# Performance work log

Hardware: AMD Instinct MI355X
Metric: run time of the kernel (lower is better)

## Reference

```python
import jax, jax.numpy as jnp
import numpy as np

B, N, F, I = 4, 1024, 32, 8
DIM, DN, NF = 256, 64, 100
H, HD = 4, 64  # heads, head_dim (H*HD == DIM)
EPS = 1e-5


def setup_inputs() -> dict:
    key = jax.random.key(0)
    ks = jax.random.split(key, 24)
    def p(k, shape, s=0.05):
        return jax.random.normal(k, shape, jnp.float32) * s
    return {
        "x": jax.random.normal(ks[0], (B, N, F, I), jnp.float32),
        "idx": jax.random.randint(ks[1], (F,), 0, NF),
        "ctx": jax.random.normal(ks[2], (B, 1, DN), jnp.float32),
        "Wp": p(ks[3], (NF, DIM * I)),          # in_projection table
        "Bp": p(ks[4], (NF, DIM)),               # feature_bias table
        "q_emb": p(ks[5], (1, DIM)),             # queries table
        "cln_kv_W": p(ks[6], (DN, 2 * DIM)), "cln_kv_b": jnp.zeros((2 * DIM,), jnp.float32),
        "cln_q_W": p(ks[7], (DN, 2 * DIM)),  "cln_q_b": jnp.zeros((2 * DIM,), jnp.float32),
        "cln_h_W": p(ks[8], (DN, 2 * DIM)),  "cln_h_b": jnp.zeros((2 * DIM,), jnp.float32),
        "Wq": p(ks[9], (DIM, DIM)), "Wk": p(ks[10], (DIM, DIM)),
        "Wv": p(ks[11], (DIM, DIM)), "Wo": p(ks[12], (DIM, DIM)),
        "W1": p(ks[13], (DIM, 4 * DIM)), "b1": jnp.zeros((4 * DIM,), jnp.float32),
        "W2": p(ks[14], (4 * DIM, DIM)), "b2": jnp.zeros((DIM,), jnp.float32),
    }


def _ln(x):
    m = x.mean(-1, keepdims=True)
    v = ((x - m) ** 2).mean(-1, keepdims=True)
    return (x - m) * jax.lax.rsqrt(v + EPS)


def _cln(x, c, W, b):
    # adaptive layernorm: ln(x) * (1 + scale(ctx)) + shift(ctx)
    h = _ln(x)
    s, sh = jnp.split(c @ W + b, 2, axis=-1)
    return h * (1.0 + s) + sh


def reference(x, idx, ctx, Wp, Bp, q_emb, cln_kv_W, cln_kv_b, cln_q_W, cln_q_b,
              cln_h_W, cln_h_b, Wq, Wk, Wv, Wo, W1, b1, W2, b2):
    b_, n_, f_, i_ = x.shape
    # gather per-feature projection weights and biases
    w = Wp[idx].reshape(f_, DIM, i_)                 # [f, d, i]
    bias = Bp[idx][None]                              # [1, f, d] (broadcasts b,n)
    kv = jnp.einsum('bnfi,fdi->bnfd', x, w)           # [b, n, f, d]
    c = ctx[:, :, None, :]                            # [b, 1, 1, dn]
    kv = _cln(kv, c, cln_kv_W, cln_kv_b) + bias
    q = jnp.broadcast_to(q_emb[None, None], (b_, n_, 1, DIM))
    # cross-attention (pre-norm, conditional)
    qn = _cln(q, c, cln_q_W, cln_q_b)
    qh = (qn @ Wq).reshape(b_, n_, 1, H, HD)
    kh = (kv @ Wk).reshape(b_, n_, f_, H, HD)
    vh = (kv @ Wv).reshape(b_, n_, f_, H, HD)
    att = jnp.einsum('bnqhe,bnfhe->bnhqf', qh, kh) / np.sqrt(HD).astype(np.float32)
    att = jax.nn.softmax(att, axis=-1)
    o = jnp.einsum('bnhqf,bnfhe->bnqhe', att, vh).reshape(b_, n_, 1, DIM) @ Wo
    h = q + o
    # MLP (pre-norm, conditional)
    hn = _cln(h, c, cln_h_W, cln_h_b)
    h = h + (jax.nn.gelu(hn @ W1 + b1) @ W2 + b2)
    return h[:, :, 0, :]                              # squeeze query dim -> [b, n, d]
```

## Files before the change

kernel.cpp:

```cpp
#include <hip/hip_runtime.h>
#include <cmath>

#define EPSV 1e-5f
using f4 = float4;

typedef __attribute__((ext_vector_type(8))) short bfrag;
typedef __attribute__((ext_vector_type(4))) float ffrag;

#define WS_SKV   0
#define WS_SHKV  1024
#define WS_SH    2048
#define WS_SHH   3072
#define WS_A     4096
#define WS_R     8192
#define WS_HT    4202496
#define WS_G     6299648
#define WS_GB    WS_G
#define WS_HNB   (WS_G + 2097152)
#define WS_W1T   (WS_G + 2621440)
#define WS_W2T   (WS_G + 2752512)

#define FMA8(acc, s, wa, wb) \
  acc[0]=fmaf((s),(wa).x,acc[0]); acc[1]=fmaf((s),(wa).y,acc[1]); \
  acc[2]=fmaf((s),(wa).z,acc[2]); acc[3]=fmaf((s),(wa).w,acc[3]); \
  acc[4]=fmaf((s),(wb).x,acc[4]); acc[5]=fmaf((s),(wb).y,acc[5]); \
  acc[6]=fmaf((s),(wb).z,acc[6]); acc[7]=fmaf((s),(wb).w,acc[7]);

#define FMA4(acc, s, wa) \
  acc[0]=fmaf((s),(wa).x,acc[0]); acc[1]=fmaf((s),(wa).y,acc[1]); \
  acc[2]=fmaf((s),(wa).z,acc[2]); acc[3]=fmaf((s),(wa).w,acc[3]);

#define DOT8(res, v, wa, wb) \
  res = fmaf((v)[0],(wa).x,res); res = fmaf((v)[1],(wa).y,res); \
  res = fmaf((v)[2],(wa).z,res); res = fmaf((v)[3],(wa).w,res); \
  res = fmaf((v)[4],(wb).x,res); res = fmaf((v)[5],(wb).y,res); \
  res = fmaf((v)[6],(wb).z,res); res = fmaf((v)[7],(wb).w,res);

__device__ __forceinline__ float bfly32(float v){
  v += __shfl_xor(v, 1);  v += __shfl_xor(v, 2);  v += __shfl_xor(v, 4);
  v += __shfl_xor(v, 8);  v += __shfl_xor(v, 16);
  return v;
}

__device__ __forceinline__ float gelu_tanh(float x){
  float inner = 0.7978845608028654f*(x + 0.044715f*x*x*x);
  return 0.5f*x*(1.0f + tanhf(inner));
}
__device__ __forceinline__ float gelu_fast(float x){
  float z2 = 1.5957691216057308f*(x + 0.044715f*x*x*x);
  return x / (1.0f + __expf(-z2));
}

__device__ __forceinline__ unsigned short f2bf(float x){
  union { float f; unsigned u; } v; v.f = x;
  unsigned r = v.u + 0x7fffu + ((v.u >> 16) & 1u);
  return (unsigned short)(r >> 16);
}

__global__ __launch_bounds__(256) void kw_conv(
  const float* __restrict__ W1, const float* __restrict__ W2,
  float* __restrict__ ws)
{
  __shared__ unsigned short lt[64][68];
  const int tid = threadIdx.x;
  int blk = blockIdx.x;
  const float* src; unsigned short* dst; int K, N, K0, N0;
  if (blk < 64){
    src = W1; dst = (unsigned short*)(ws + WS_W1T);
    K = 256; N = 1024; K0 = (blk >> 4)*64; N0 = (blk & 15)*64;
  } else {
    blk -= 64;
    src = W2; dst = (unsigned short*)(ws + WS_W2T);
    K = 1024; N = 256; K0 = (blk >> 2)*64; N0 = (blk & 3)*64;
  }
  #pragma unroll
  for (int i=0;i<4;++i){
    int r = i*16 + (tid>>4);
    int c = (tid&15)*4;
    f4 v = *(const f4*)(src + (size_t)(K0+r)*N + N0 + c);
    lt[r][c]   = f2bf(v.x); lt[r][c+1] = f2bf(v.y);
    lt[r][c+2] = f2bf(v.z); lt[r][c+3] = f2bf(v.w);
  }
  __syncthreads();
  #pragma unroll
  for (int i=0;i<4;++i){
    int n  = i*16 + (tid>>4);
    int kc = (tid&15)*4;
    ushort4 u;
    u.x = lt[kc][n]; u.y = lt[kc+1][n]; u.z = lt[kc+2][n]; u.w = lt[kc+3][n];
    *(ushort4*)(dst + (size_t)(N0+n)*K + K0 + kc) = u;
  }
}

__global__ __launch_bounds__(256) void k0_all(
    const float* __restrict__ ctx, const float* __restrict__ q_emb,
    const float* __restrict__ Wkv, const float* __restrict__ bkv,
    const float* __restrict__ Wqc, const float* __restrict__ bqc,
    const float* __restrict__ Whc, const float* __restrict__ bhc,
    const float* __restrict__ Wq,  const float* __restrict__ Wk,
    float* __restrict__ ws)
{
  const int b = blockIdx.x >> 2, h = blockIdx.x & 3;
  const int tid = threadIdx.x;
  __shared__ float c[64], qn[256], ph[256], qh64[64], red[8];
  if (tid < 64) c[tid] = ctx[b*64 + tid];
  __syncthreads();

  float skv = bkv[tid],      shkv = bkv[256+tid];
  float sq  = bqc[tid],      shq  = bqc[256+tid];
  float sh  = bhc[tid],      shh  = bhc[256+tid];
  #pragma unroll 8
  for (int j=0;j<64;++j){
    float cj = c[j];
    skv  = fmaf(cj, Wkv[j*512 + tid],       skv);
    shkv = fmaf(cj, Wkv[j*512 + 256 + tid], shkv);
    sq   = fmaf(cj, Wqc[j*512 + tid],       sq);
    shq  = fmaf(cj, Wqc[j*512 + 256 + tid], shq);
    sh   = fmaf(cj, Whc[j*512 + tid],       sh);
    shh  = fmaf(cj, Whc[j*512 + 256 + tid], shh);
  }
  if (h == 0){
    ws[WS_SKV  + b*256 + tid] = skv;
    ws[WS_SHKV + b*256 + tid] = shkv;
    ws[WS_SH   + b*256 + tid] = sh;
    ws[WS_SHH  + b*256 + tid] = shh;
  }

  float qe = q_emb[tid];
  float s1r = qe, s2r = qe*qe;
  for (int mm=1;mm<64;mm<<=1){ s1r += __shfl_xor(s1r,mm); s2r += __shfl_xor(s2r,mm); }
  int wv = tid>>6, ln = tid&63;
  if (ln==0){ red[wv*2]=s1r; red[wv*2+1]=s2r; }
  __syncthreads();
  float S1 = red[0]+red[2]+red[4]+red[6];
  float S2 = red[1]+red[3]+red[5]+red[7];
  float mean = S1*(1.0f/256.0f);
  float var  = S2*(1.0f/256.0f) - mean*mean;
  float rs   = rsqrtf(var + EPSV);
  qn[tid] = (qe-mean)*rs*(1.0f+sq) + shq;
  __syncthreads();

  {
    const int t = tid & 63, ks = tid >> 6;
    float p = 0.f;
    const float* wq = Wq + (size_t)(ks*64)*256 + h*64 + t;
    #pragma unroll 8
    for (int d=0; d<64; ++d) p = fmaf(qn[ks*64+d], wq[d*256], p);
    ph[tid] = p;
  }
  __syncthreads();
  if (tid < 64) qh64[tid] = ph[tid] + ph[64+tid] + ph[128+tid] + ph[192+tid];
  __syncthreads();

  {
    float a = 0.f;
    const float* wkr = Wk + (size_t)tid*256 + h*64;
    #pragma unroll
    for (int e4=0; e4<16; ++e4){
      f4 wv4 = *(const f4*)(wkr + e4*4);
      a = fmaf(qh64[e4*4+0], wv4.x, a);
      a = fmaf(qh64[e4*4+1], wv4.y, a);
      a = fmaf(qh64[e4*4+2], wv4.z, a);
      a = fmaf(qh64[e4*4+3], wv4.w, a);
    }
    ws[WS_A + b*1024 + h*256 + tid] = 0.125f*a;
  }
}

__global__ __launch_bounds__(256) void k1f_attn(
  const float* __restrict__ x, const int* __restrict__ idx,
  const float* __restrict__ Wp, const float* __restrict__ Bp,
  float* __restrict__ ws)
{
  __shared__ float xs[2048];
  __shared__ float wls[2][2048];
  __shared__ float As[1024];

  const int tid = threadIdx.x;
  const int p0  = blockIdx.x * 8;
  const int b   = p0 >> 10;
  const int t   = tid >> 5;
  const int dg  = tid & 31;
  const int dA  = 4*dg, dB = 128 + 4*dg;

  {
    const float* xg = x + (size_t)p0*256 + tid*8;
    f4 a  = *(const f4*)xg;
    f4 bq = *(const f4*)(xg + 4);
    *(f4*)&xs[tid*8]     = a;
    *(f4*)&xs[tid*8 + 4] = bq;
  }
  *(f4*)&As[tid*4] = *(const f4*)(ws + WS_A + b*1024 + tid*4);

  f4 skA = *(const f4*)(ws + WS_SKV  + b*256 + dA);
  f4 skB = *(const f4*)(ws + WS_SKV  + b*256 + dB);
  f4 shA = *(const f4*)(ws + WS_SHKV + b*256 + dA);
  f4 shB = *(const f4*)(ws + WS_SHKV + b*256 + dB);
  float coef[8] = {1.f+skA.x,1.f+skA.y,1.f+skA.z,1.f+skA.w,
                   1.f+skB.x,1.f+skB.y,1.f+skB.z,1.f+skB.w};
  float shk[8]  = {shA.x,shA.y,shA.z,shA.w, shB.x,shB.y,shB.z,shB.w};

  int row = idx[0];
  f4 u0, u1;
  {
    const float* wp0 = Wp + (size_t)row*2048 + tid*8;
    u0 = *(const f4*)wp0;
    u1 = *(const f4*)(wp0 + 4);
  }

  float l[4] = {0.f,0.f,0.f,0.f};
  float racc[4][8] = {};

  for (int f = 0; f < 32; ++f){
    {
      float* wb = wls[f&1];
      wb[0*256+tid]=u0.x; wb[1*256+tid]=u0.y; wb[2*256+tid]=u0.z; wb[3*256+tid]=u0.w;
      wb[4*256+tid]=u1.x; wb[5*256+tid]=u1.y; wb[6*256+tid]=u1.z; wb[7*256+tid]=u1.w;
    }
    f4 ba = *(const f4*)(Bp + (size_t)row*256 + dA);
    f4 bb = *(const f4*)(Bp + (size_t)row*256 + dB);
    int rown = idx[f < 31 ? f+1 : 31];
    const float* wpn = Wp + (size_t)rown*2048 + tid*8;
    row = rown;
    __syncthreads();
    u0 = *(const f4*)wpn;
    u1 = *(const f4*)(wpn + 4);

    f4 xa = *(const f4*)&xs[t*256 + f*8];
    f4 xb = *(const f4*)&xs[t*256 + f*8 + 4];
    float xf[8] = {xa.x,xa.y,xa.z,xa.w, xb.x,xb.y,xb.z,xb.w};

    float val[8] = {};
    const float* wrow = wls[f&1];
    #pragma unroll
    for (int i=0;i<8;++i){
      f4 wa = *(const f4*)&wrow[i*256 + dA];
      f4 wbv = *(const f4*)&wrow[i*256 + dB];
      FMA8(val, xf[i], wa, wbv);
    }

    float s=0.f, ss=0.f;
    #pragma unroll
    for (int jj=0;jj<8;++jj){ s += val[jj]; ss = fmaf(val[jj],val[jj],ss); }
    s = bfly32(s); ss = bfly32(ss);
    float mean = s*(1.f/256.f);
    float var  = ss*(1.f/256.f) - mean*mean;
    float rsg  = rsqrtf(var + EPSV);
    float mrs  = mean*rsg;

    float off[8] = {shk[0]+ba.x, shk[1]+ba.y, shk[2]+ba.z, shk[3]+ba.w,
                    shk[4]+bb.x, shk[5]+bb.y, shk[6]+bb.z, shk[7]+bb.w};
    float kvl[8];
    #pragma unroll
    for (int jj=0;jj<8;++jj)
      kvl[jj] = fmaf(fmaf(val[jj], rsg, -mrs), coef[jj], off[jj]);

    #pragma unroll
    for (int h=0;h<4;++h){
      f4 Aa = *(const f4*)&As[h*256 + dA];
      f4 Ab = *(const f4*)&As[h*256 + dB];
      float lg = 0.f;
      DOT8(lg, kvl, Aa, Ab);
      lg = bfly32(lg);
      float pp = __expf(lg);
      l[h] += pp;
      #pragma unroll
      for (int jj=0;jj<8;++jj)
        racc[h][jj] = fmaf(pp, kvl[jj], racc[h][jj]);
    }
  }

  float* rp = ws + WS_R + (size_t)(p0+t)*1024;
  #pragma unroll
  for (int h=0;h<4;++h){
    float inv = 1.f / l[h];
    *(f4*)&rp[h*256 + dA] = make_float4(racc[h][0]*inv, racc[h][1]*inv,
                                        racc[h][2]*inv, racc[h][3]*inv);
    *(f4*)&rp[h*256 + dB] = make_float4(racc[h][4]*inv, racc[h][5]*inv,
                                        racc[h][6]*inv, racc[h][7]*inv);
  }
}

__global__ __launch_bounds__(256) void k2_ovo(
  const float* __restrict__ Wv, const float* __restrict__ Wo,
  const float* __restrict__ q_emb, float* __restrict__ ws)
{
  __shared__ float rl[8192];
  __shared__ float ot[2048];
  __shared__ float wt[2][2048];

  const int tid = threadIdx.x;
  const int p0  = blockIdx.x * 8;
  const int b   = p0 >> 10;
  const int tq  = tid >> 5;
  const int jq  = tid & 31;
  const int cA  = 4*jq, cB = 128 + 4*jq;
  const int hA  = jq >> 4, hB = 2 + (jq >> 4);

  #pragma unroll
  for (int i=0;i<8;++i){
    int off = i*1024 + tid*4;
    *(f4*)&rl[off] = *(const f4*)(ws + WS_R + (size_t)p0*1024 + off);
  }

  const int q0 = tid, q1 = tid + 256;
  f4 uw0, uw1;
  uw0 = *(const f4*)(Wv + (size_t)(q0>>6)*256 + (q0&63)*4);
  uw1 = *(const f4*)(Wv + (size_t)(q1>>6)*256 + (q1&63)*4);

  float oa[8] = {};
  for (int c=0; c<32; ++c){
    float* wb = wt[c&1];
    *(f4*)&wb[(q0>>6)*256 + (q0&63)*4] = uw0;
    *(f4*)&wb[(q1>>6)*256 + (q1&63)*4] = uw1;
    __syncthreads();
    int cn = (c < 31) ? c+1 : 31;
    uw0 = *(const f4*)(Wv + (size_t)(cn*8 + (q0>>6))*256 + (q0&63)*4);
    uw1 = *(const f4*)(Wv + (size_t)(cn*8 + (q1>>6))*256 + (q1&63)*4);
    const float* wrow = wt[c&1];
    #pragma unroll
    for (int dd=0; dd<8; ++dd){
      int d = c*8 + dd;
      float rA = rl[tq*1024 + hA*256 + d];
      float rB = rl[tq*1024 + hB*256 + d];
      f4 w0 = *(const f4*)&wrow[dd*256 + cA];
      f4 w1 = *(const f4*)&wrow[dd*256 + cB];
      FMA4(oa, rA, w0);
      float* ob4 = oa + 4;
      FMA4(ob4, rB, w1);
    }
  }
  *(f4*)&ot[tq*256 + cA] = make_float4(oa[0],oa[1],oa[2],oa[3]);
  *(f4*)&ot[tq*256 + cB] = make_float4(oa[4],oa[5],oa[6],oa[7]);
  uw0 = *(const f4*)(Wo + (size_t)(q0>>6)*256 + (q0&63)*4);
  uw1 = *(const f4*)(Wo + (size_t)(q1>>6)*256 + (q1&63)*4);
  __syncthreads();

  float ob[8] = {};
  for (int c=0; c<32; ++c){
    float* wb = wt[c&1];
    *(f4*)&wb[(q0>>6)*256 + (q0&63)*4] = uw0;
    *(f4*)&wb[(q1>>6)*256 + (q1&63)*4] = uw1;
    __syncthreads();
    int cn = (c < 31) ? c+1 : 31;
    uw0 = *(const f4*)(Wo + (size_t)(cn*8 + (q0>>6))*256 + (q0&63)*4);
    uw1 = *(const f4*)(Wo + (size_t)(cn*8 + (q1>>6))*256 + (q1&63)*4);
    const float* wrow = wt[c&1];
    #pragma unroll
    for (int dd=0; dd<8; ++dd){
      int cc = c*8 + dd;
      float a = ot[tq*256 + cc];
      f4 w0 = *(const f4*)&wrow[dd*256 + cA];
      f4 w1 = *(const f4*)&wrow[dd*256 + cB];
      FMA8(ob, a, w0, w1);
    }
  }

  f4 qA = *(const f4*)(q_emb + cA);
  f4 qB = *(const f4*)(q_emb + cB);
  float ht[8] = {ob[0]+qA.x, ob[1]+qA.y, ob[2]+qA.z, ob[3]+qA.w,
                 ob[4]+qB.x, ob[5]+qB.y, ob[6]+qB.z, ob[7]+qB.w};
  float s=0.f, ss=0.f;
  #pragma unroll
  for (int jj=0;jj<8;++jj){ s += ht[jj]; ss = fmaf(ht[jj],ht[jj],ss); }
  s = bfly32(s); ss = bfly32(ss);
  float mean = s*(1.f/256.f);
  float var  = ss*(1.f/256.f) - mean*mean;
  float rsg  = rsqrtf(var + EPSV);
  f4 sH0 = *(const f4*)(ws + WS_SH  + b*256 + cA);
  f4 sH1 = *(const f4*)(ws + WS_SH  + b*256 + cB);
  f4 hH0 = *(const f4*)(ws + WS_SHH + b*256 + cA);
  f4 hH1 = *(const f4*)(ws + WS_SHH + b*256 + cB);
  float sHv[8]  = {sH0.x,sH0.y,sH0.z,sH0.w, sH1.x,sH1.y,sH1.z,sH1.w};
  float hHv[8]  = {hH0.x,hH0.y,hH0.z,hH0.w, hH1.x,hH1.y,hH1.z,hH1.w};
  float hnv[8];
  #pragma unroll
  for (int jj=0;jj<8;++jj)
    hnv[jj] = (ht[jj]-mean)*rsg*(1.f+sHv[jj]) + hHv[jj];

  float* htp = ws + WS_HT + (size_t)(p0+tq)*256;
  *(f4*)(htp+cA) = make_float4(ht[0],ht[1],ht[2],ht[3]);
  *(f4*)(htp+cB) = make_float4(ht[4],ht[5],ht[6],ht[7]);
  unsigned short* hnb = (unsigned short*)(ws + WS_HNB);
  ushort4 uA, uB;
  uA.x=f2bf(hnv[0]); uA.y=f2bf(hnv[1]); uA.z=f2bf(hnv[2]); uA.w=f2bf(hnv[3]);
  uB.x=f2bf(hnv[4]); uB.y=f2bf(hnv[5]); uB.z=f2bf(hnv[6]); uB.w=f2bf(hnv[7]);
  *(ushort4*)(hnb + (size_t)(p0+tq)*256 + cA) = uA;
  *(ushort4*)(hnb + (size_t)(p0+tq)*256 + cB) = uB;
}

__global__ __launch_bounds__(256) void k3_mfma(
  const float* __restrict__ b1, float* __restrict__ ws)
{
  __shared__ unsigned short aT[2][64*40];
  __shared__ unsigned short bT[2][128*40];
  const unsigned short* hnb = (const unsigned short*)(ws + WS_HNB);
  const unsigned short* w1t = (const unsigned short*)(ws + WS_W1T);
  unsigned short* gb = (unsigned short*)(ws + WS_GB);

  const int tid = threadIdx.x;
  const int M0 = (blockIdx.x >> 3) * 64;
  const int N0 = (blockIdx.x & 7) * 128;
  const int lane = tid & 63;
  const int wid = tid >> 6;
  const int wm = wid >> 1, wn = wid & 1;
  const int m16 = lane & 15, q = lane >> 4;

  const int sa_m = tid >> 2, sa_k = (tid & 3) * 8;
  const int sb_n = tid >> 1, sb_k = (tid & 1) * 16;

  f4 ua, ub0, ub1;
  ua  = *(const f4*)(hnb + (size_t)(M0 + sa_m)*256 + sa_k);
  ub0 = *(const f4*)(w1t + (size_t)(N0 + sb_n)*256 + sb_k);
  ub1 = *(const f4*)(w1t + (size_t)(N0 + sb_n)*256 + sb_k + 8);

  ffrag acc[2][4];
  #pragma unroll
  for (int i=0;i<2;++i)
    #pragma unroll
    for (int j=0;j<4;++j) acc[i][j] = (ffrag){0.f,0.f,0.f,0.f};

  for (int ks=0; ks<8; ++ks){
    const int buf = ks & 1;
    *(f4*)&aT[buf][sa_m*40 + sa_k]     = ua;
    *(f4*)&bT[buf][sb_n*40 + sb_k]     = ub0;
    *(f4*)&bT[buf][sb_n*40 + sb_k + 8] = ub1;
    __syncthreads();
    int kn = (ks < 7) ? ks+1 : 7;
    ua  = *(const f4*)(hnb + (size_t)(M0 + sa_m)*256 + kn*32 + sa_k);
    ub0 = *(const f4*)(w1t + (size_t)(N0 + sb_n)*256 + kn*32 + sb_k);
    ub1 = *(const f4*)(w1t + (size_t)(N0 + sb_n)*256 + kn*32 + sb_k + 8);

    bfrag af[2], bf_[4];
    af[0] = *(const bfrag*)&aT[buf][(wm*32 + m16)*40 + q*8];
    af[1] = *(const bfrag*)&aT[buf][(wm*32 + 16 + m16)*40 + q*8];
    #pragma unroll
    for (int j=0;j<4;++j)
      bf_[j] = *(const bfrag*)&bT[buf][(wn*64 + j*16 + m16)*40 + q*8];
    #pragma unroll
    for (int i=0;i<2;++i)
      #pragma unroll
      for (int j=0;j<4;++j)
        acc[i][j] = __builtin_amdgcn_mfma_f32_16x16x32_bf16(bf_[j], af[i], acc[i][j], 0, 0, 0);
  }

  #pragma unroll
  for (int i=0;i<2;++i){
    const int m = M0 + wm*32 + i*16 + m16;
    #pragma unroll
    for (int j=0;j<4;++j){
      const int n4 = N0 + wn*64 + j*16 + q*4;
      f4 bv = *(const f4*)(b1 + n4);
      ushort4 u;
      u.x = f2bf(gelu_fast(acc[i][j][0] + bv.x));
      u.y = f2bf(gelu_fast(acc[i][j][1] + bv.y));
      u.z = f2bf(gelu_fast(acc[i][j][2] + bv.z));
      u.w = f2bf(gelu_fast(acc[i][j][3] + bv.w));
      *(ushort4*)(gb + (size_t)m*1024 + n4) = u;
    }
  }
}

__global__ __launch_bounds__(256) void k4_mfma(
  const float* __restrict__ b2, const float* __restrict__ ws_c,
  float* __restrict__ ws, float* __restrict__ out)
{
  __shared__ unsigned short aT[2][32*40];
  __shared__ unsigned short bT[2][64*40];
  const unsigned short* gb  = (const unsigned short*)(ws_c + WS_GB);
  const unsigned short* w2t = (const unsigned short*)(ws_c + WS_W2T);

  const int tid = threadIdx.x;
  const int M0 = (blockIdx.x >> 2) * 32;
  const int N0 = (blockIdx.x & 3) * 64;
  const int lane = tid & 63;
  const int wid = tid >> 6;
  const int wm = wid >> 1, wn = wid & 1;
  const int m16 = lane & 15, q = lane >> 4;

  const int sa_m = tid >> 3, sa_k = (tid & 7) * 4;
  const int sb_n = tid >> 2, sb_k = (tid & 3) * 8;

  ushort4 ua;
  f4 ub;
  ua = *(const ushort4*)(gb  + (size_t)(M0 + sa_m)*1024 + sa_k);
  ub = *(const f4*)(w2t + (size_t)(N0 + sb_n)*1024 + sb_k);

  ffrag acc[2];
  acc[0] = (ffrag){0.f,0.f,0.f,0.f};
  acc[1] = (ffrag){0.f,0.f,0.f,0.f};

  for (int ks=0; ks<32; ++ks){
    const int buf = ks & 1;
    *(ushort4*)&aT[buf][sa_m*40 + sa_k] = ua;
    *(f4*)&bT[buf][sb_n*40 + sb_k]      = ub;
    __syncthreads();
    int kn = (ks < 31) ? ks+1 : 31;
    ua = *(const ushort4*)(gb  + (size_t)(M0 + sa_m)*1024 + kn*32 + sa_k);
    ub = *(const f4*)(w2t + (size_t)(N0 + sb_n)*1024 + kn*32 + sb_k);

    bfrag af, bf0, bf1;
    af  = *(const bfrag*)&aT[buf][(wm*16 + m16)*40 + q*8];
    bf0 = *(const bfrag*)&bT[buf][(wn*32 + m16)*40 + q*8];
    bf1 = *(const bfrag*)&bT[buf][(wn*32 + 16 + m16)*40 + q*8];
    acc[0] = __builtin_amdgcn_mfma_f32_16x16x32_bf16(bf0, af, acc[0], 0, 0, 0);
    acc[1] = __builtin_amdgcn_mfma_f32_16x16x32_bf16(bf1, af, acc[1], 0, 0, 0);
  }

  const int m = M0 + wm*16 + m16;
  #pragma unroll
  for (int j=0;j<2;++j){
    const int n4 = N0 + wn*32 + j*16 + q*4;
    f4 bv = *(const f4*)(b2 + n4);
    f4 hv = *(const f4*)(ws + WS_HT + (size_t)m*256 + n4);
    *(f4*)(out + (size_t)m*256 + n4) =
      make_float4(acc[j][0]+bv.x+hv.x, acc[j][1]+bv.y+hv.y,
                  acc[j][2]+bv.z+hv.z, acc[j][3]+bv.w+hv.w);
  }
}

extern "C" void kernel_launch(void* const* d_in, const int* in_sizes, int n_in,
                              void* d_out, int out_size, void* d_ws, size_t ws_size,
                              hipStream_t stream)
{
  const float* x    = (const float*)d_in[0];
  const int*   idx  = (const int*)  d_in[1];
  const float* ctx  = (const float*)d_in[2];
  const float* Wp   = (const float*)d_in[3];
  const float* Bp   = (const float*)d_in[4];
  const float* qemb = (const float*)d_in[5];
  const float* Wkv  = (const float*)d_in[6];
  const float* bkv  = (const float*)d_in[7];
  const float* Wqc  = (const float*)d_in[8];
  const float* bqc  = (const float*)d_in[9];
  const float* Whc  = (const float*)d_in[10];
  const float* bhc  = (const float*)d_in[11];
  const float* Wq   = (const float*)d_in[12];
  const float* Wk   = (const float*)d_in[13];
  const float* Wv   = (const float*)d_in[14];
  const float* Wo   = (const float*)d_in[15];
  const float* W1   = (const float*)d_in[16];
  const float* b1   = (const float*)d_in[17];
  const float* W2   = (const float*)d_in[18];
  const float* b2   = (const float*)d_in[19];
  float* ws  = (float*)d_ws;
  float* out = (float*)d_out;

  hipLaunchKernelGGL(kw_conv,  dim3(128), dim3(256), 0, stream, W1, W2, ws);
  hipLaunchKernelGGL(k0_all,   dim3(16),  dim3(256), 0, stream,
                     ctx, qemb, Wkv, bkv, Wqc, bqc, Whc, bhc, Wq, Wk, ws);
  hipLaunchKernelGGL(k1f_attn, dim3(512), dim3(256), 0, stream, x, idx, Wp, Bp, ws);
  hipLaunchKernelGGL(k2_ovo,   dim3(512), dim3(256), 0, stream, Wv, Wo, qemb, ws);
  hipLaunchKernelGGL(k3_mfma,  dim3(512), dim3(256), 0, stream, b1, ws);
  hipLaunchKernelGGL(k4_mfma,  dim3(512), dim3(256), 0, stream, b2, ws, ws, out);
}
```

Baseline: 217.7 us.

## Fold Wv·Wo into per-head matrix, split attention over features, use MFMA GEMM

```diff
diff --git a/kernel.cpp b/kernel.cpp
--- a/kernel.cpp
+++ b/kernel.cpp
@@ -14,11 +14,13 @@
 #define WS_A     4096
 #define WS_R     8192
 #define WS_HT    4202496
+#define WS_L     5251072
 #define WS_G     6299648
 #define WS_GB    WS_G
 #define WS_HNB   (WS_G + 2097152)
 #define WS_W1T   (WS_G + 2621440)
 #define WS_W2T   (WS_G + 2752512)
+#define WS_MT    (WS_G + 2883584)
 
 #define FMA8(acc, s, wa, wb) \
   acc[0]=fmaf((s),(wa).x,acc[0]); acc[1]=fmaf((s),(wa).y,acc[1]); \
@@ -26,10 +28,6 @@
   acc[4]=fmaf((s),(wb).x,acc[4]); acc[5]=fmaf((s),(wb).y,acc[5]); \
   acc[6]=fmaf((s),(wb).z,acc[6]); acc[7]=fmaf((s),(wb).w,acc[7]);
 
-#define FMA4(acc, s, wa) \
-  acc[0]=fmaf((s),(wa).x,acc[0]); acc[1]=fmaf((s),(wa).y,acc[1]); \
-  acc[2]=fmaf((s),(wa).z,acc[2]); acc[3]=fmaf((s),(wa).w,acc[3]);
-
 #define DOT8(res, v, wa, wb) \
   res = fmaf((v)[0],(wa).x,res); res = fmaf((v)[1],(wa).y,res); \
   res = fmaf((v)[2],(wa).z,res); res = fmaf((v)[3],(wa).w,res); \
@@ -42,10 +40,6 @@
   return v;
 }
 
-__device__ __forceinline__ float gelu_tanh(float x){
-  float inner = 0.7978845608028654f*(x + 0.044715f*x*x*x);
-  return 0.5f*x*(1.0f + tanhf(inner));
-}
 __device__ __forceinline__ float gelu_fast(float x){
   float z2 = 1.5957691216057308f*(x + 0.044715f*x*x*x);
   return x / (1.0f + __expf(-z2));
@@ -55,6 +49,11 @@
   union { float f; unsigned u; } v; v.f = x;
   unsigned r = v.u + 0x7fffu + ((v.u >> 16) & 1u);
   return (unsigned short)(r >> 16);
+}
+__device__ __forceinline__ void bf2x(unsigned u, float& a, float& b){
+  union { unsigned u; float f; } x, y;
+  x.u = u << 16; y.u = u & 0xffff0000u;
+  a = x.f; b = y.f;
 }
 
 __global__ __launch_bounds__(256) void kw_conv(
@@ -90,6 +89,41 @@
     u.x = lt[kc][n]; u.y = lt[kc+1][n]; u.z = lt[kc+2][n]; u.w = lt[kc+3][n];
     *(ushort4*)(dst + (size_t)(N0+n)*K + K0 + kc) = u;
   }
+}
+
+__global__ __launch_bounds__(256) void km_conv(
+  const float* __restrict__ Wv, const float* __restrict__ Wo,
+  float* __restrict__ ws)
+{
+  __shared__ float wvs[4*64];
+  __shared__ float wos[64*256];
+  const int tid = threadIdx.x;
+  const int h   = blockIdx.x >> 6;
+  const int dg4 = blockIdx.x & 63;
+  {
+    int d = tid >> 6, e = tid & 63;
+    wvs[d*64+e] = Wv[(size_t)(dg4*4 + d)*256 + h*64 + e];
+  }
+  {
+    int e = tid >> 2, c = (tid & 3)*64;
+    const float* src = Wo + (size_t)(h*64 + e)*256 + c;
+    #pragma unroll
+    for (int i=0;i<16;++i)
+      *(f4*)&wos[e*256 + c + i*4] = *(const f4*)(src + i*4);
+  }
+  __syncthreads();
+  float acc[4] = {};
+  for (int e=0;e<64;++e){
+    float wo = wos[e*256 + tid];
+    acc[0] = fmaf(wvs[0*64+e], wo, acc[0]);
+    acc[1] = fmaf(wvs[1*64+e], wo, acc[1]);
+    acc[2] = fmaf(wvs[2*64+e], wo, acc[2]);
+    acc[3] = fmaf(wvs[3*64+e], wo, acc[3]);
+  }
+  unsigned short* Mt = (unsigned short*)(ws + WS_MT);
+  ushort4 u;
+  u.x = f2bf(acc[0]); u.y = f2bf(acc[1]); u.z = f2bf(acc[2]); u.w = f2bf(acc[3]);
+  *(ushort4*)(Mt + (size_t)tid*1024 + h*256 + dg4*4) = u;
 }
 
 __global__ __launch_bounds__(256) void k0_all(
@@ -167,17 +201,19 @@
   }
 }
 
-__global__ __launch_bounds__(256) void k1f_attn(
+__global__ __launch_bounds__(256,4) void k1f_attn(
   const float* __restrict__ x, const int* __restrict__ idx,
   const float* __restrict__ Wp, const float* __restrict__ Bp,
   float* __restrict__ ws)
 {
   __shared__ float xs[2048];
-  __shared__ float wls[2][2048];
+  __shared__ float wls[4096];
   __shared__ float As[1024];
 
   const int tid = threadIdx.x;
-  const int p0  = blockIdx.x * 8;
+  const int p0  = (blockIdx.x >> 1) * 8;
+  const int half= blockIdx.x & 1;
+  const int f0  = half * 16;
   const int b   = p0 >> 10;
   const int t   = tid >> 5;
   const int dg  = tid & 31;
@@ -200,166 +236,206 @@
                    1.f+skB.x,1.f+skB.y,1.f+skB.z,1.f+skB.w};
   float shk[8]  = {shA.x,shA.y,shA.z,shA.w, shB.x,shB.y,shB.z,shB.w};
 
-  int row = idx[0];
-  f4 u0, u1;
-  {
-    const float* wp0 = Wp + (size_t)row*2048 + tid*8;
-    u0 = *(const f4*)wp0;
-    u1 = *(const f4*)(wp0 + 4);
-  }
+  int r0 = idx[f0], r1 = idx[f0+1];
+  f4 u0 = *(const f4*)(Wp + (size_t)r0*2048 + tid*8);
+  f4 u1 = *(const f4*)(Wp + (size_t)r0*2048 + tid*8 + 4);
+  f4 u2 = *(const f4*)(Wp + (size_t)r1*2048 + tid*8);
+  f4 u3 = *(const f4*)(Wp + (size_t)r1*2048 + tid*8 + 4);
 
   float l[4] = {0.f,0.f,0.f,0.f};
   float racc[4][8] = {};
 
-  for (int f = 0; f < 32; ++f){
-    {
-      float* wb = wls[f&1];
-      wb[0*256+tid]=u0.x; wb[1*256+tid]=u0.y; wb[2*256+tid]=u0.z; wb[3*256+tid]=u0.w;
-      wb[4*256+tid]=u1.x; wb[5*256+tid]=u1.y; wb[6*256+tid]=u1.z; wb[7*256+tid]=u1.w;
-    }
-    f4 ba = *(const f4*)(Bp + (size_t)row*256 + dA);
-    f4 bb = *(const f4*)(Bp + (size_t)row*256 + dB);
-    int rown = idx[f < 31 ? f+1 : 31];
-    const float* wpn = Wp + (size_t)rown*2048 + tid*8;
-    row = rown;
+  for (int fi = 0; fi < 8; ++fi){
+    const int f = f0 + fi*2;
     __syncthreads();
-    u0 = *(const f4*)wpn;
-    u1 = *(const f4*)(wpn + 4);
-
-    f4 xa = *(const f4*)&xs[t*256 + f*8];
-    f4 xb = *(const f4*)&xs[t*256 + f*8 + 4];
-    float xf[8] = {xa.x,xa.y,xa.z,xa.w, xb.x,xb.y,xb.z,xb.w};
-
-    float val[8] = {};
-    const float* wrow = wls[f&1];
-    #pragma unroll
-    for (int i=0;i<8;++i){
-      f4 wa = *(const f4*)&wrow[i*256 + dA];
-      f4 wbv = *(const f4*)&wrow[i*256 + dB];
-      FMA8(val, xf[i], wa, wbv);
-    }
-
-    float s=0.f, ss=0.f;
-    #pragma unroll
-    for (int jj=0;jj<8;++jj){ s += val[jj]; ss = fmaf(val[jj],val[jj],ss); }
-    s = bfly32(s); ss = bfly32(ss);
-    float mean = s*(1.f/256.f);
-    float var  = ss*(1.f/256.f) - mean*mean;
-    float rsg  = rsqrtf(var + EPSV);
-    float mrs  = mean*rsg;
-
-    float off[8] = {shk[0]+ba.x, shk[1]+ba.y, shk[2]+ba.z, shk[3]+ba.w,
-                    shk[4]+bb.x, shk[5]+bb.y, shk[6]+bb.z, shk[7]+bb.w};
-    float kvl[8];
-    #pragma unroll
-    for (int jj=0;jj<8;++jj)
-      kvl[jj] = fmaf(fmaf(val[jj], rsg, -mrs), coef[jj], off[jj]);
-
-    #pragma unroll
-    for (int h=0;h<4;++h){
-      f4 Aa = *(const f4*)&As[h*256 + dA];
-      f4 Ab = *(const f4*)&As[h*256 + dB];
-      float lg = 0.f;
-      DOT8(lg, kvl, Aa, Ab);
-      lg = bfly32(lg);
-      float pp = __expf(lg);
-      l[h] += pp;
+    wls[0*256+tid]=u0.x; wls[1*256+tid]=u0.y; wls[2*256+tid]=u0.z; wls[3*256+tid]=u0.w;
+    wls[4*256+tid]=u1.x; wls[5*256+tid]=u1.y; wls[6*256+tid]=u1.z; wls[7*256+tid]=u1.w;
+    wls[2048+0*256+tid]=u2.x; wls[2048+1*256+tid]=u2.y;
+    wls[2048+2*256+tid]=u2.z; wls[2048+3*256+tid]=u2.w;
+    wls[2048+4*256+tid]=u3.x; wls[2048+5*256+tid]=u3.y;
+    wls[2048+6*256+tid]=u3.z; wls[2048+7*256+tid]=u3.w;
+    __syncthreads();
+
+    f4 ba0 = *(const f4*)(Bp + (size_t)r0*256 + dA);
+    f4 bb0 = *(const f4*)(Bp + (size_t)r0*256 + dB);
+    f4 ba1 = *(const f4*)(Bp + (size_t)r1*256 + dA);
+    f4 bb1 = *(const f4*)(Bp + (size_t)r1*256 + dB);
+
+    const int fn = (fi < 7) ? f + 2 : f0;
+    int rn0 = idx[fn], rn1 = idx[fn+1];
+    u0 = *(const f4*)(Wp + (size_t)rn0*2048 + tid*8);
+    u1 = *(const f4*)(Wp + (size_t)rn0*2048 + tid*8 + 4);
+    u2 = *(const f4*)(Wp + (size_t)rn1*2048 + tid*8);
+    u3 = *(const f4*)(Wp + (size_t)rn1*2048 + tid*8 + 4);
+
+    #pragma unroll
+    for (int sub=0; sub<2; ++sub){
+      const float* wrow = wls + sub*2048;
+      const int fc = f + sub;
+      f4 ba = sub ? ba1 : ba0;
+      f4 bb = sub ? bb1 : bb0;
+
+      f4 xa = *(const f4*)&xs[t*256 + fc*8];
+      f4 xb = *(const f4*)&xs[t*256 + fc*8 + 4];
+      float xf[8] = {xa.x,xa.y,xa.z,xa.w, xb.x,xb.y,xb.z,xb.w};
+
+      float val[8] = {};
+      #pragma unroll
+      for (int i=0;i<8;++i){
+        f4 wa  = *(const f4*)&wrow[i*256 + dA];
+        f4 wbv = *(const f4*)&wrow[i*256 + dB];
+        FMA8(val, xf[i], wa, wbv);
+      }
+
+      float s=0.f, ss=0.f;
+      #pragma unroll
+      for (int jj=0;jj<8;++jj){ s += val[jj]; ss = fmaf(val[jj],val[jj],ss); }
+      s = bfly32(s); ss = bfly32(ss);
+      float mean = s*(1.f/256.f);
+      float var  = ss*(1.f/256.f) - mean*mean;
+      float rsg  = rsqrtf(var + EPSV);
+      float mrs  = mean*rsg;
+
+      float off[8] = {shk[0]+ba.x, shk[1]+ba.y, shk[2]+ba.z, shk[3]+ba.w,
+                      shk[4]+bb.x, shk[5]+bb.y, shk[6]+bb.z, shk[7]+bb.w};
+      float kvl[8];
       #pragma unroll
       for (int jj=0;jj<8;++jj)
-        racc[h][jj] = fmaf(pp, kvl[jj], racc[h][jj]);
+        kvl[jj] = fmaf(fmaf(val[jj], rsg, -mrs), coef[jj], off[jj]);
+
+      #pragma unroll
+      for (int h=0;h<4;++h){
+        f4 Aa = *(const f4*)&As[h*256 + dA];
+        f4 Ab = *(const f4*)&As[h*256 + dB];
+        float lg = 0.f;
+        DOT8(lg, kvl, Aa, Ab);
+        lg = bfly32(lg);
+        float pp = __expf(lg);
+        l[h] += pp;
+        #pragma unroll
+        for (int jj=0;jj<8;++jj)
+          racc[h][jj] = fmaf(pp, kvl[jj], racc[h][jj]);
+      }
     }
-  }
-
-  float* rp = ws + WS_R + (size_t)(p0+t)*1024;
+    r0 = rn0; r1 = rn1;
+  }
+
+  unsigned short* Pr = (unsigned short*)(ws + WS_R);
+  size_t base = (size_t)(half*4096 + p0 + t) * 1024;
   #pragma unroll
   for (int h=0;h<4;++h){
-    float inv = 1.f / l[h];
-    *(f4*)&rp[h*256 + dA] = make_float4(racc[h][0]*inv, racc[h][1]*inv,
-                                        racc[h][2]*inv, racc[h][3]*inv);
-    *(f4*)&rp[h*256 + dB] = make_float4(racc[h][4]*inv, racc[h][5]*inv,
-                                        racc[h][6]*inv, racc[h][7]*inv);
-  }
-}
-
-__global__ __launch_bounds__(256) void k2_ovo(
-  const float* __restrict__ Wv, const float* __restrict__ Wo,
+    ushort4 ua, ub;
+    ua.x=f2bf(racc[h][0]); ua.y=f2bf(racc[h][1]); ua.z=f2bf(racc[h][2]); ua.w=f2bf(racc[h][3]);
+    ub.x=f2bf(racc[h][4]); ub.y=f2bf(racc[h][5]); ub.z=f2bf(racc[h][6]); ub.w=f2bf(racc[h][7]);
+    *(ushort4*)(Pr + base + h*256 + dA) = ua;
+    *(ushort4*)(Pr + base + h*256 + dB) = ub;
+  }
+  if (dg == 0){
+    float* Lp = ws + WS_L;
+    #pragma unroll
+    for (int h=0;h<4;++h) Lp[(size_t)(half*4096 + p0 + t)*4 + h] = l[h];
+  }
+}
+
+__global__ __launch_bounds__(256) void kc_comb(float* __restrict__ ws)
+{
+  unsigned short* Pr = (unsigned short*)(ws + WS_R);
+  const float* Lp = ws + WS_L;
+  const int tid = threadIdx.x;
+  const int p0 = blockIdx.x * 8;
+  #pragma unroll
+  for (int k=0;k<4;++k){
+    size_t e0 = (size_t)p0*1024 + (size_t)k*2048 + (size_t)tid*8;
+    int t = (int)(e0 >> 10);
+    int h = (int)((e0 >> 8) & 3);
+    float inv = 1.f / (Lp[(size_t)t*4 + h] + Lp[(size_t)(4096 + t)*4 + h]);
+    uint4 a  = *(const uint4*)(Pr + e0);
+    uint4 bq = *(const uint4*)(Pr + 4194304 + e0);
+    unsigned au[4] = {a.x, a.y, a.z, a.w};
+    unsigned bu[4] = {bq.x, bq.y, bq.z, bq.w};
+    unsigned r[4];
+    #pragma unroll
+    for (int i=0;i<4;++i){
+      float alo, ahi, blo, bhi;
+      bf2x(au[i], alo, ahi);
+      bf2x(bu[i], blo, bhi);
+      float lo = (alo + blo) * inv;
+      float hi = (ahi + bhi) * inv;
+      r[i] = ((unsigned)f2bf(hi) << 16) | (unsigned)f2bf(lo);
+    }
+    *(uint4*)(Pr + e0) = make_uint4(r[0], r[1], r[2], r[3]);
+  }
+}
+
+__global__ __launch_bounds__(256) void k2g_mfma(float* __restrict__ ws)
+{
+  __shared__ unsigned short aT[2][32*40];
+  __shared__ unsigned short bT[2][64*40];
+  const unsigned short* rb = (const unsigned short*)(ws + WS_R);
+  const unsigned short* mt = (const unsigned short*)(ws + WS_MT);
+
+  const int tid = threadIdx.x;
+  const int M0 = (blockIdx.x >> 2) * 32;
+  const int N0 = (blockIdx.x & 3) * 64;
+  const int lane = tid & 63;
+  const int wid = tid >> 6;
+  const int wm = wid >> 1, wn = wid & 1;
+  const int m16 = lane & 15, q = lane >> 4;
+
+  const int sa_m = tid >> 3, sa_k = (tid & 7) * 4;
+  const int sb_n = tid >> 2, sb_k = (tid & 3) * 8;
+
+  ushort4 ua;
+  f4 ub;
+  ua = *(const ushort4*)(rb + (size_t)(M0 + sa_m)*1024 + sa_k);
+  ub = *(const f4*)(mt + (size_t)(N0 + sb_n)*1024 + sb_k);
+
+  ffrag acc[2];
+  acc[0] = (ffrag){0.f,0.f,0.f,0.f};
+  acc[1] = (ffrag){0.f,0.f,0.f,0.f};
+
+  for (int ks=0; ks<32; ++ks){
+    const int buf = ks & 1;
+    *(ushort4*)&aT[buf][sa_m*40 + sa_k] = ua;
+    *(f4*)&bT[buf][sb_n*40 + sb_k]      = ub;
+    __syncthreads();
+    int kn = (ks < 31) ? ks+1 : 31;
+    ua = *(const ushort4*)(rb + (size_t)(M0 + sa_m)*1024 + kn*32 + sa_k);
+    ub = *(const f4*)(mt + (size_t)(N0 + sb_n)*1024 + kn*32 + sb_k);
+
+    bfrag af, bf0, bf1;
+    af  = *(const bfrag*)&aT[buf][(wm*16 + m16)*40 + q*8];
+    bf0 = *(const bfrag*)&bT[buf][(wn*32 + m16)*40 + q*8];
+    bf1 = *(const bfrag*)&bT[buf][(wn*32 + 16 + m16)*40 + q*8];
+    acc[0] = __builtin_amdgcn_mfma_f32_16x16x32_bf16(bf0, af, acc[0], 0, 0, 0);
+    acc[1] = __builtin_amdgcn_mfma_f32_16x16x32_bf16(bf1, af, acc[1], 0, 0, 0);
+  }
+
+  const int m = M0 + wm*16 + m16;
+  #pragma unroll
+  for (int j=0;j<2;++j){
+    const int n4 = N0 + wn*32 + j*16 + q*4;
+    *(f4*)(ws + WS_HT + (size_t)m*256 + n4) =
+      make_float4(acc[j][0], acc[j][1], acc[j][2], acc[j][3]);
+  }
+}
+
+__global__ __launch_bounds__(256) void ke_ln(
   const float* __restrict__ q_emb, float* __restrict__ ws)
 {
-  __shared__ float rl[8192];
-  __shared__ float ot[2048];
-  __shared__ float wt[2][2048];
-
-  const int tid = threadIdx.x;
-  const int p0  = blockIdx.x * 8;
-  const int b   = p0 >> 10;
-  const int tq  = tid >> 5;
-  const int jq  = tid & 31;
-  const int cA  = 4*jq, cB = 128 + 4*jq;
-  const int hA  = jq >> 4, hB = 2 + (jq >> 4);
-
-  #pragma unroll
-  for (int i=0;i<8;++i){
-    int off = i*1024 + tid*4;
-    *(f4*)&rl[off] = *(const f4*)(ws + WS_R + (size_t)p0*1024 + off);
-  }
-
-  const int q0 = tid, q1 = tid + 256;
-  f4 uw0, uw1;
-  uw0 = *(const f4*)(Wv + (size_t)(q0>>6)*256 + (q0&63)*4);
-  uw1 = *(const f4*)(Wv + (size_t)(q1>>6)*256 + (q1&63)*4);
-
-  float oa[8] = {};
-  for (int c=0; c<32; ++c){
-    float* wb = wt[c&1];
-    *(f4*)&wb[(q0>>6)*256 + (q0&63)*4] = uw0;
-    *(f4*)&wb[(q1>>6)*256 + (q1&63)*4] = uw1;
-    __syncthreads();
-    int cn = (c < 31) ? c+1 : 31;
-    uw0 = *(const f4*)(Wv + (size_t)(cn*8 + (q0>>6))*256 + (q0&63)*4);
-    uw1 = *(const f4*)(Wv + (size_t)(cn*8 + (q1>>6))*256 + (q1&63)*4);
-    const float* wrow = wt[c&1];
-    #pragma unroll
-    for (int dd=0; dd<8; ++dd){
-      int d = c*8 + dd;
-      float rA = rl[tq*1024 + hA*256 + d];
-      float rB = rl[tq*1024 + hB*256 + d];
-      f4 w0 = *(const f4*)&wrow[dd*256 + cA];
-      f4 w1 = *(const f4*)&wrow[dd*256 + cB];
-      FMA4(oa, rA, w0);
-      float* ob4 = oa + 4;
-      FMA4(ob4, rB, w1);
-    }
-  }
-  *(f4*)&ot[tq*256 + cA] = make_float4(oa[0],oa[1],oa[2],oa[3]);
-  *(f4*)&ot[tq*256 + cB] = make_float4(oa[4],oa[5],oa[6],oa[7]);
-  uw0 = *(const f4*)(Wo + (size_t)(q0>>6)*256 + (q0&63)*4);
-  uw1 = *(const f4*)(Wo + (size_t)(q1>>6)*256 + (q1&63)*4);
-  __syncthreads();
-
-  float ob[8] = {};
-  for (int c=0; c<32; ++c){
-    float* wb = wt[c&1];
-    *(f4*)&wb[(q0>>6)*256 + (q0&63)*4] = uw0;
-    *(f4*)&wb[(q1>>6)*256 + (q1&63)*4] = uw1;
-    __syncthreads();
-    int cn = (c < 31) ? c+1 : 31;
-    uw0 = *(const f4*)(Wo + (size_t)(cn*8 + (q0>>6))*256 + (q0&63)*4);
-    uw1 = *(const f4*)(Wo + (size_t)(cn*8 + (q1>>6))*256 + (q1&63)*4);
-    const float* wrow = wt[c&1];
-    #pragma unroll
-    for (int dd=0; dd<8; ++dd){
-      int cc = c*8 + dd;
-      float a = ot[tq*256 + cc];
-      f4 w0 = *(const f4*)&wrow[dd*256 + cA];
-      f4 w1 = *(const f4*)&wrow[dd*256 + cB];
-      FMA8(ob, a, w0, w1);
-    }
-  }
-
+  const int tid = threadIdx.x;
+  const int p0 = blockIdx.x * 8;
+  const int b  = p0 >> 10;
+  const int tq = tid >> 5, jq = tid & 31;
+  const int cA = 4*jq, cB = 128 + 4*jq;
+
+  float* op = ws + WS_HT + (size_t)(p0+tq)*256;
+  f4 oA = *(const f4*)(op + cA);
+  f4 oB = *(const f4*)(op + cB);
   f4 qA = *(const f4*)(q_emb + cA);
   f4 qB = *(const f4*)(q_emb + cB);
-  float ht[8] = {ob[0]+qA.x, ob[1]+qA.y, ob[2]+qA.z, ob[3]+qA.w,
-                 ob[4]+qB.x, ob[5]+qB.y, ob[6]+qB.z, ob[7]+qB.w};
+  float ht[8] = {oA.x+qA.x, oA.y+qA.y, oA.z+qA.z, oA.w+qA.w,
+                 oB.x+qB.x, oB.y+qB.y, oB.z+qB.z, oB.w+qB.w};
   float s=0.f, ss=0.f;
   #pragma unroll
   for (int jj=0;jj<8;++jj){ s += ht[jj]; ss = fmaf(ht[jj],ht[jj],ss); }
@@ -378,9 +454,8 @@
   for (int jj=0;jj<8;++jj)
     hnv[jj] = (ht[jj]-mean)*rsg*(1.f+sHv[jj]) + hHv[jj];
 
-  float* htp = ws + WS_HT + (size_t)(p0+tq)*256;
-  *(f4*)(htp+cA) = make_float4(ht[0],ht[1],ht[2],ht[3]);
-  *(f4*)(htp+cB) = make_float4(ht[4],ht[5],ht[6],ht[7]);
+  *(f4*)(op+cA) = make_float4(ht[0],ht[1],ht[2],ht[3]);
+  *(f4*)(op+cB) = make_float4(ht[4],ht[5],ht[6],ht[7]);
   unsigned short* hnb = (unsigned short*)(ws + WS_HNB);
   ushort4 uA, uB;
   uA.x=f2bf(hnv[0]); uA.y=f2bf(hnv[1]); uA.z=f2bf(hnv[2]); uA.w=f2bf(hnv[3]);
@@ -546,11 +621,14 @@
   float* ws  = (float*)d_ws;
   float* out = (float*)d_out;
 
-  hipLaunchKernelGGL(kw_conv,  dim3(128), dim3(256), 0, stream, W1, W2, ws);
-  hipLaunchKernelGGL(k0_all,   dim3(16),  dim3(256), 0, stream,
+  hipLaunchKernelGGL(kw_conv,  dim3(128),  dim3(256), 0, stream, W1, W2, ws);
+  hipLaunchKernelGGL(km_conv,  dim3(256),  dim3(256), 0, stream, Wv, Wo, ws);
+  hipLaunchKernelGGL(k0_all,   dim3(16),   dim3(256), 0, stream,
                      ctx, qemb, Wkv, bkv, Wqc, bqc, Whc, bhc, Wq, Wk, ws);
-  hipLaunchKernelGGL(k1f_attn, dim3(512), dim3(256), 0, stream, x, idx, Wp, Bp, ws);
-  hipLaunchKernelGGL(k2_ovo,   dim3(512), dim3(256), 0, stream, Wv, Wo, qemb, ws);
-  hipLaunchKernelGGL(k3_mfma,  dim3(512), dim3(256), 0, stream, b1, ws);
-  hipLaunchKernelGGL(k4_mfma,  dim3(512), dim3(256), 0, stream, b2, ws, ws, out);
-}
+  hipLaunchKernelGGL(k1f_attn, dim3(1024), dim3(256), 0, stream, x, idx, Wp, Bp, ws);
+  hipLaunchKernelGGL(kc_comb,  dim3(512),  dim3(256), 0, stream, ws);
+  hipLaunchKernelGGL(k2g_mfma, dim3(512),  dim3(256), 0, stream, ws);
+  hipLaunchKernelGGL(ke_ln,    dim3(512),  dim3(256), 0, stream, qemb, ws);
+  hipLaunchKernelGGL(k3_mfma,  dim3(512),  dim3(256), 0, stream, b1, ws);
+  hipLaunchKernelGGL(k4_mfma,  dim3(512),  dim3(256), 0, stream, b2, ws, ws, out);
+}
```

New measurement: 202.7 us. 6.9% less time.
